# Optimization experiments

Hardware: AMD Instinct MI355X
Metric: run time of the kernel (lower is better)

## Reference

```python
import jax, jax.numpy as jnp
import numpy as np

D_MODEL = 1024
NUM_HEADS = 16
D_K = D_MODEL // NUM_HEADS


def setup_inputs() -> dict:
    key = jax.random.key(0)
    ks = jax.random.split(key, 12)
    B, S = 1, 4096
    s = 1.0 / np.sqrt(D_MODEL)
    inp = {
        'query': jax.random.normal(ks[0], (B, S, D_MODEL), jnp.float32),
        'key': jax.random.normal(ks[1], (B, S, D_MODEL), jnp.float32),
        'value': jax.random.normal(ks[2], (B, S, D_MODEL), jnp.float32),
        'W_q': jax.random.normal(ks[3], (D_MODEL, D_MODEL), jnp.float32) * s,
        'b_q': jnp.zeros((D_MODEL,), jnp.float32),
        'W_k': jax.random.normal(ks[4], (D_MODEL, D_MODEL), jnp.float32) * s,
        'b_k': jnp.zeros((D_MODEL,), jnp.float32),
        'W_v': jax.random.normal(ks[5], (D_MODEL, D_MODEL), jnp.float32) * s,
        'b_v': jnp.zeros((D_MODEL,), jnp.float32),
        'W_o': jax.random.normal(ks[6], (D_MODEL, D_MODEL), jnp.float32) * s,
        'b_o': jnp.zeros((D_MODEL,), jnp.float32),
    }
    return inp


def reference(query, key, value, W_q, b_q, W_k, b_k, W_v, b_v, W_o, b_o):
    B, S, _ = query.shape
    # torch nn.Linear: y = x @ W.T + b
    Q = query @ W_q.T + b_q
    K = key @ W_k.T + b_k
    V = value @ W_v.T + b_v
    # (B, S, H, d_k) -> (B, H, S, d_k)
    Q = Q.reshape(B, S, NUM_HEADS, D_K).transpose(0, 2, 1, 3)
    K = K.reshape(B, S, NUM_HEADS, D_K).transpose(0, 2, 1, 3)
    V = V.reshape(B, S, NUM_HEADS, D_K).transpose(0, 2, 1, 3)
    scale = 1.0 / jnp.sqrt(jnp.asarray(D_K, Q.dtype))
    qk = jnp.einsum('bhqd,bhkd->bhqk', Q, K) * scale  # [B,H,S,S]
    attn = jax.nn.softmax(qk, axis=-1)
    out = jnp.einsum('bhqk,bhkd->bhqd', attn, V)
    out = out.transpose(0, 2, 1, 3).reshape(B, S, D_MODEL)
    return out @ W_o.T + b_o
```

## Files before the change

### kernel.cpp

```cpp
#include <hip/hip_runtime.h>
#include <cstdint>
#include <cstddef>

typedef __bf16 bf16_t;
typedef _Float16 f16_t;
typedef __attribute__((ext_vector_type(8))) __bf16 bf16x8;
typedef __attribute__((ext_vector_type(4))) __bf16 bf16x4;
typedef __attribute__((ext_vector_type(2))) __bf16 bf16x2;
typedef __attribute__((ext_vector_type(8))) _Float16 f16x8;
typedef __attribute__((ext_vector_type(2))) _Float16 f16x2;
typedef __attribute__((ext_vector_type(4))) float floatx4;
typedef __attribute__((ext_vector_type(2))) float floatx2;
typedef __attribute__((ext_vector_type(16))) float floatx16;
typedef __attribute__((ext_vector_type(2))) int i32x2;

#define S_LEN 4096
#define DM 1024
#define NH 16
#define DKH 64
#define NSPLIT 4
#define KT_PER (S_LEN / 64 / NSPLIT)

#define QSCALE 0.1803368801111601f

__device__ __forceinline__ void async_b128(void* lds, const void* g) {
    __builtin_amdgcn_global_load_lds(
        (__attribute__((address_space(1))) void*)(uintptr_t)g,
        (__attribute__((address_space(3))) void*)lds,
        16, 0, 0);
}

__device__ __forceinline__ void fence_all() { __builtin_amdgcn_s_waitcnt(0); }

__device__ __forceinline__ floatx4 mfma16(bf16x8 a, bf16x8 b, floatx4 c) {
    return __builtin_amdgcn_mfma_f32_16x16x32_bf16(a, b, c, 0, 0, 0);
}
__device__ __forceinline__ floatx16 mfma32(bf16x8 a, bf16x8 b, floatx16 c) {
    return __builtin_amdgcn_mfma_f32_32x32x16_bf16(a, b, c, 0, 0, 0);
}
__device__ __forceinline__ int f2i(float x) { return __builtin_bit_cast(int, x); }
__device__ __forceinline__ float i2f(int x) { return __builtin_bit_cast(float, x); }
__device__ __forceinline__ int p2i(bf16x2 x) { return __builtin_bit_cast(int, x); }

__global__ __launch_bounds__(256) void convert_all_kernel(
    const float* __restrict__ q, const float* __restrict__ k,
    const float* __restrict__ v, const float* __restrict__ wqf,
    const float* __restrict__ wkf, const float* __restrict__ wvf,
    const float* __restrict__ wof, bf16_t* __restrict__ dst_in,
    bf16_t* __restrict__ dst_w) {
    const size_t i = ((size_t)blockIdx.x * 256 + threadIdx.x) * 4;
    const float* s;
    bf16_t* d;
    size_t off;
    if (i < 12582912) {
        const int r = (int)(i >> 22);
        s = (r == 0) ? q : (r == 1) ? k : v;
        off = i & 4194303;
        d = dst_in + (size_t)r * 4194304 + off;
    } else {
        const size_t j = i - 12582912;
        const int r = (int)(j >> 20);
        s = (r == 0) ? wqf : (r == 1) ? wkf : (r == 2) ? wvf : wof;
        off = j & 1048575;
        d = dst_w + (size_t)r * 1048576 + off;
    }
    const floatx4 val = *(const floatx4*)(s + off);
    bf16x4 o;
    o[0] = (bf16_t)val[0]; o[1] = (bf16_t)val[1];
    o[2] = (bf16_t)val[2]; o[3] = (bf16_t)val[3];
    *(bf16x4*)d = o;
}

template <int BN, typename OutT, bool TRANSC>
__device__ __forceinline__ void gemm_bt_body(const bf16_t* __restrict__ A,
                                             const bf16_t* __restrict__ B,
                                             const float* __restrict__ bias,
                                             OutT* __restrict__ C, float oscale) {
    constexpr int K = 1024, N = 1024, BK = 64;
    constexpr int NT = BN / 32;
    __shared__ bf16_t As[128 * BK];
    __shared__ bf16_t Bs[BN * BK];
    const int tid = threadIdx.x;
    const int wid = tid >> 6, lane = tid & 63;
    const int quad = lane >> 4, l16 = lane & 15;
    const int m0 = blockIdx.y * 128, n0 = blockIdx.x * BN;
    const int wm = (wid & 1) * 64, wn = (wid >> 1) * (BN / 2);

    floatx4 acc[4][NT] = {};

    for (int k0 = 0; k0 < K; k0 += BK) {
        __syncthreads();
#pragma unroll
        for (int i = 0; i < (128 * BK) / 2048; ++i) {
            const int c = (i << 8) + tid;
            const int row = c >> 3;
            const int ko = (c & 7) << 3;
            const int lb = ((i << 8) + (wid << 6)) << 3;
            async_b128(&As[lb], A + (size_t)(m0 + row) * K + k0 + ko);
        }
#pragma unroll
        for (int i = 0; i < (BN * BK) / 2048; ++i) {
            const int c = (i << 8) + tid;
            const int row = c >> 3;
            const int ko = (c & 7) << 3;
            const int lb = ((i << 8) + (wid << 6)) << 3;
            async_b128(&Bs[lb], B + (size_t)(n0 + row) * K + k0 + ko);
        }
        fence_all();
        __syncthreads();

#pragma unroll
        for (int kk = 0; kk < 2; ++kk) {
            bf16x8 af[4], bfr[NT];
#pragma unroll
            for (int t = 0; t < 4; ++t)
                af[t] = *(const bf16x8*)&As[(wm + t * 16 + l16) * BK + kk * 32 + quad * 8];
#pragma unroll
            for (int t = 0; t < NT; ++t)
                bfr[t] = *(const bf16x8*)&Bs[(wn + t * 16 + l16) * BK + kk * 32 + quad * 8];
#pragma unroll
            for (int mt = 0; mt < 4; ++mt)
#pragma unroll
                for (int nt = 0; nt < NT; ++nt)
                    acc[mt][nt] = mfma16(af[mt], bfr[nt], acc[mt][nt]);
        }
    }

#pragma unroll
    for (int mt = 0; mt < 4; ++mt)
#pragma unroll
        for (int nt = 0; nt < NT; ++nt) {
            const int col = n0 + wn + nt * 16 + l16;
            const float bv = bias[col];
            if constexpr (TRANSC) {
                const int row0 = m0 + wm + mt * 16 + quad * 4;
                bf16x4 o;
#pragma unroll
                for (int r = 0; r < 4; ++r)
                    o[r] = (bf16_t)((acc[mt][nt][r] + bv) * oscale);
                *(bf16x4*)&C[(size_t)col * S_LEN + row0] = o;
            } else {
#pragma unroll
                for (int r = 0; r < 4; ++r) {
                    const int row = m0 + wm + mt * 16 + quad * 4 + r;
                    C[(size_t)row * N + col] = (OutT)((acc[mt][nt][r] + bv) * oscale);
                }
            }
        }
}

__global__ __launch_bounds__(256) void gemm_qkv_kernel(
    const bf16_t* __restrict__ qx, const bf16_t* __restrict__ kx,
    const bf16_t* __restrict__ vx, const bf16_t* __restrict__ wq,
    const bf16_t* __restrict__ wk, const bf16_t* __restrict__ wv,
    const float* __restrict__ bq, const float* __restrict__ bk,
    const float* __restrict__ bv, bf16_t* __restrict__ Qp,
    bf16_t* __restrict__ Kp, bf16_t* __restrict__ Vt) {
    const int z = blockIdx.z;
    const bf16_t* A = (z == 0) ? qx : (z == 1) ? kx : vx;
    const bf16_t* B = (z == 0) ? wq : (z == 1) ? wk : wv;
    const float* bias = (z == 0) ? bq : (z == 1) ? bk : bv;
    if (z == 2) {
        gemm_bt_body<128, bf16_t, true>(A, B, bias, Vt, 1.0f);
    } else {
        bf16_t* C = (z == 0) ? Qp : Kp;
        gemm_bt_body<128, bf16_t, false>(A, B, bias, C, (z == 0) ? QSCALE : 1.0f);
    }
}

__global__ __launch_bounds__(256) void gemm_out_kernel(
    const bf16_t* __restrict__ AO, const bf16_t* __restrict__ wo,
    const float* __restrict__ bo, float* __restrict__ out) {
    gemm_bt_body<64, float, false>(AO, wo, bo, out, 1.0f);
}

__global__ __launch_bounds__(256, 2) void flash_kernel(
    const bf16_t* __restrict__ Q, const bf16_t* __restrict__ K,
    const bf16_t* __restrict__ Vt, f16_t* __restrict__ Opart,
    float* __restrict__ Lpart) {
    __shared__ bf16_t smem[16384];
    bf16_t* Ks = smem;
    bf16_t* Vs = smem + 8192;

    const int tid = threadIdx.x;
    const int wave = tid >> 6, lane = tid & 63;
    const int h32 = lane >> 5, c = lane & 31;
    const int head = blockIdx.y;
    const int sp = blockIdx.z;
    const int qbase = blockIdx.x * 256 + wave * 64;
    const int kv0 = sp * (S_LEN / NSPLIT);

    bf16x8 Qf[2][4];
#pragma unroll
    for (int nt = 0; nt < 2; ++nt)
#pragma unroll
        for (int s = 0; s < 4; ++s)
            Qf[nt][s] = *(const bf16x8*)(Q + (size_t)(qbase + nt * 32 + c) * DM +
                                         head * DKH + s * 16 + h32 * 8);

    floatx16 oa[2][2] = {};
    floatx2 la2[2][2] = {};

    const bf16_t* kptr = K + (size_t)(kv0 + lane) * DM + head * DKH + wave * 16;
    const bf16_t* vptr = Vt + (size_t)(head * DKH + lane) * S_LEN + kv0 + wave * 16;
    bf16_t* ksl = Ks + wave * 1024;
    bf16_t* vsl = Vs + wave * 1024;

    async_b128(ksl, kptr);       async_b128(ksl + 512, kptr + 8);
    async_b128(vsl, vptr);       async_b128(vsl + 512, vptr + 8);
    kptr += 64 * DM; vptr += 64;

    for (int kt = 0; kt < KT_PER; ++kt) {
        const int buf = kt & 1;
        fence_all();
        __syncthreads();
        if (kt + 1 < KT_PER) {
            bf16_t* kd = ksl + (buf ^ 1) * 4096;
            bf16_t* vd = vsl + (buf ^ 1) * 4096;
            async_b128(kd, kptr);     async_b128(kd + 512, kptr + 8);
            async_b128(vd, vptr);     async_b128(vd + 512, vptr + 8);
            kptr += 64 * DM; vptr += 64;
        }

        bf16x8 Kf[2][4];
#pragma unroll
        for (int mt = 0; mt < 2; ++mt)
#pragma unroll
            for (int s = 0; s < 4; ++s)
                Kf[mt][s] = *(const bf16x8*)&Ks[buf * 4096 + ((2 * s + h32) * 64 + mt * 32 + c) * 8];

        floatx16 sc[2][2];
#pragma unroll
        for (int mt = 0; mt < 2; ++mt)
#pragma unroll
            for (int nt = 0; nt < 2; ++nt)
#pragma unroll
                for (int j = 0; j < 16; ++j)
                    sc[mt][nt][j] = -3.0f;

#pragma unroll
        for (int s = 0; s < 4; ++s)
#pragma unroll
            for (int mt = 0; mt < 2; ++mt)
#pragma unroll
                for (int nt = 0; nt < 2; ++nt)
                    sc[mt][nt] = mfma32(Kf[mt][s], Qf[nt][s], sc[mt][nt]);

        bf16x8 Vf[2][4];
#pragma unroll
        for (int dt = 0; dt < 2; ++dt)
#pragma unroll
            for (int s = 0; s < 4; ++s)
                Vf[dt][s] = *(const bf16x8*)&Vs[buf * 4096 + ((2 * s + h32) * 64 + dt * 32 + c) * 8];

#pragma unroll
        for (int nt = 0; nt < 2; ++nt) {
            int pk[2][8];
#pragma unroll
            for (int mt = 0; mt < 2; ++mt)
#pragma unroll
                for (int rr = 0; rr < 8; ++rr) {
                    const float p0 = __builtin_amdgcn_exp2f(sc[mt][nt][2 * rr]);
                    const float p1 = __builtin_amdgcn_exp2f(sc[mt][nt][2 * rr + 1]);
                    la2[nt][rr & 1] += floatx2{p0, p1};
                    bf16x2 w; w[0] = (bf16_t)p0; w[1] = (bf16_t)p1;
                    pk[mt][rr] = p2i(w);
                }
#pragma unroll
            for (int s = 0; s < 4; ++s) {
                const int a = s >> 1, b4 = (s & 1) * 4;
                const i32x2 r02 = __builtin_amdgcn_permlane32_swap(
                    pk[a][b4 + 0], pk[a][b4 + 2], false, false);
                const i32x2 r13 = __builtin_amdgcn_permlane32_swap(
                    pk[a][b4 + 1], pk[a][b4 + 3], false, false);
                union { bf16x8 v; int d[4]; } P;
                P.d[0] = r02[0];
                P.d[1] = r13[0];
                P.d[2] = r02[1];
                P.d[3] = r13[1];
                oa[0][nt] = mfma32(Vf[0][s], P.v, oa[0][nt]);
                oa[1][nt] = mfma32(Vf[1][s], P.v, oa[1][nt]);
            }
        }
    }

#pragma unroll
    for (int nt = 0; nt < 2; ++nt) {
        float t = la2[nt][0][0] + la2[nt][0][1] + la2[nt][1][0] + la2[nt][1][1];
        t += i2f(__shfl_xor(f2i(t), 32));
        if (h32 == 0)
            Lpart[(size_t)(sp * NH + head) * S_LEN + qbase + nt * 32 + c] = t;
    }

    fence_all();
    __syncthreads();
    f16_t* ot = (f16_t*)smem + wave * (32 * 72);
#pragma unroll
    for (int nt = 0; nt < 2; ++nt) {
#pragma unroll
        for (int dt = 0; dt < 2; ++dt)
#pragma unroll
            for (int rr = 0; rr < 8; ++rr) {
                const int d0 = dt * 32 + ((2 * rr) & 3) + 8 * (rr >> 1) + 4 * h32;
                f16x2 w;
                w[0] = (f16_t)oa[dt][nt][2 * rr];
                w[1] = (f16_t)oa[dt][nt][2 * rr + 1];
                *(f16x2*)&ot[c * 72 + d0] = w;
            }
        fence_all();
        __syncthreads();
        const int r = lane & 31;
#pragma unroll
        for (int j = 0; j < 4; ++j) {
            const f16x8 v = *(const f16x8*)&ot[r * 72 + h32 * 32 + j * 8];
            *(f16x8*)(Opart + ((size_t)sp * S_LEN + qbase + nt * 32 + r) * DM +
                      head * DKH + h32 * 32 + j * 8) = v;
        }
        fence_all();
        __syncthreads();
    }
}

__global__ __launch_bounds__(256) void reduce_kernel(
    const f16_t* __restrict__ Op, const float* __restrict__ Lp,
    bf16_t* __restrict__ AO) {
    const size_t f = ((size_t)blockIdx.x * 256 + threadIdx.x) * 8;
    const int q = (int)(f >> 10);
    const int h = (int)((f & 1023) >> 6);
    float l = 0.f;
#pragma unroll
    for (int sp = 0; sp < NSPLIT; ++sp)
        l += Lp[(size_t)(sp * NH + h) * S_LEN + q];
    const float inv = 1.0f / l;
    float s[8] = {};
#pragma unroll
    for (int sp = 0; sp < NSPLIT; ++sp) {
        const f16x8 v = *(const f16x8*)(Op + (size_t)sp * (S_LEN * DM) + f);
#pragma unroll
        for (int j = 0; j < 8; ++j) s[j] += (float)v[j];
    }
    bf16x8 o;
#pragma unroll
    for (int j = 0; j < 8; ++j) o[j] = (bf16_t)(s[j] * inv);
    *(bf16x8*)(AO + f) = o;
}

extern "C" void kernel_launch(void* const* d_in, const int* in_sizes, int n_in,
                              void* d_out, int out_size, void* d_ws, size_t ws_size,
                              hipStream_t stream) {
    const float* q  = (const float*)d_in[0];
    const float* k  = (const float*)d_in[1];
    const float* v  = (const float*)d_in[2];
    const float* Wq = (const float*)d_in[3];
    const float* bq = (const float*)d_in[4];
    const float* Wk = (const float*)d_in[5];
    const float* bk = (const float*)d_in[6];
    const float* Wv = (const float*)d_in[7];
    const float* bv = (const float*)d_in[8];
    const float* Wo = (const float*)d_in[9];
    const float* bo = (const float*)d_in[10];
    float* out = (float*)d_out;

    bf16_t* ws = (bf16_t*)d_ws;
    bf16_t* qx = ws;
    bf16_t* kx = qx + 4194304;
    bf16_t* vx = kx + 4194304;
    bf16_t* spare = vx + 4194304;
    f16_t*  Opart = (f16_t*)ws;
    bf16_t* wq = spare + 4194304;
    bf16_t* wk = wq + 1048576;
    bf16_t* wv = wk + 1048576;
    bf16_t* wo = wv + 1048576;
    bf16_t* Qp = wo + 1048576;
    bf16_t* Kp = Qp + 4194304;
    bf16_t* Vt = Kp + 4194304;
    bf16_t* AO = Vt + 4194304;
    float*  Lpart = (float*)(AO + 4194304);

    convert_all_kernel<<<dim3(16384), 256, 0, stream>>>(q, k, v, Wq, Wk, Wv, Wo,
                                                        qx, wq);
    gemm_qkv_kernel<<<dim3(8, 32, 3), 256, 0, stream>>>(qx, kx, vx, wq, wk, wv,
                                                        bq, bk, bv, Qp, Kp, Vt);
    flash_kernel<<<dim3(16, 16, NSPLIT), 256, 0, stream>>>(Qp, Kp, Vt, Opart, Lpart);
    reduce_kernel<<<dim3(2048), 256, 0, stream>>>(Opart, Lpart, AO);
    gemm_out_kernel<<<dim3(16, 32), 256, 0, stream>>>(AO, wo, bo, out);
    (void)in_sizes; (void)n_in; (void)out_size; (void)ws_size;
}
```

Measured before the change: 268.9 us.

## Fuse fp32-to-bf16 input conversion into QKV GEMM tile loads

Removes the separate pass that converted the query/key/value activations to bf16. The QKV GEMM now loads fp32 tiles straight into LDS, using an XOR swizzle to avoid bank conflicts, and converts them to bf16 in registers before the MFMA. The K tile shrinks from 64 to 32 for every GEMM so the fp32 A tile fits in LDS, which doubles the number of barrier and load rounds per GEMM. Only the weights are still converted in a separate, smaller kernel.

```diff
diff --git a/kernel.cpp b/kernel.cpp
--- a/kernel.cpp
+++ b/kernel.cpp
@@ -42,43 +42,33 @@
 __device__ __forceinline__ float i2f(int x) { return __builtin_bit_cast(float, x); }
 __device__ __forceinline__ int p2i(bf16x2 x) { return __builtin_bit_cast(int, x); }
 
-__global__ __launch_bounds__(256) void convert_all_kernel(
-    const float* __restrict__ q, const float* __restrict__ k,
-    const float* __restrict__ v, const float* __restrict__ wqf,
-    const float* __restrict__ wkf, const float* __restrict__ wvf,
-    const float* __restrict__ wof, bf16_t* __restrict__ dst_in,
+__global__ __launch_bounds__(256) void convert_w_kernel(
+    const float* __restrict__ wqf, const float* __restrict__ wkf,
+    const float* __restrict__ wvf, const float* __restrict__ wof,
     bf16_t* __restrict__ dst_w) {
     const size_t i = ((size_t)blockIdx.x * 256 + threadIdx.x) * 4;
-    const float* s;
-    bf16_t* d;
-    size_t off;
-    if (i < 12582912) {
-        const int r = (int)(i >> 22);
-        s = (r == 0) ? q : (r == 1) ? k : v;
-        off = i & 4194303;
-        d = dst_in + (size_t)r * 4194304 + off;
-    } else {
-        const size_t j = i - 12582912;
-        const int r = (int)(j >> 20);
-        s = (r == 0) ? wqf : (r == 1) ? wkf : (r == 2) ? wvf : wof;
-        off = j & 1048575;
-        d = dst_w + (size_t)r * 1048576 + off;
-    }
+    const int r = (int)(i >> 20);
+    const float* s = (r == 0) ? wqf : (r == 1) ? wkf : (r == 2) ? wvf : wof;
+    const size_t off = i & 1048575;
     const floatx4 val = *(const floatx4*)(s + off);
     bf16x4 o;
     o[0] = (bf16_t)val[0]; o[1] = (bf16_t)val[1];
     o[2] = (bf16_t)val[2]; o[3] = (bf16_t)val[3];
-    *(bf16x4*)d = o;
-}
-
-template <int BN, typename OutT, bool TRANSC>
-__device__ __forceinline__ void gemm_bt_body(const bf16_t* __restrict__ A,
+    *(bf16x4*)(dst_w + (size_t)r * 1048576 + off) = o;
+}
+
+template <int BN, typename OutT, bool TRANSC, typename AT>
+__device__ __forceinline__ void gemm_bt_body(const AT* __restrict__ A,
                                              const bf16_t* __restrict__ B,
                                              const float* __restrict__ bias,
                                              OutT* __restrict__ C, float oscale) {
-    constexpr int K = 1024, N = 1024, BK = 64;
+    constexpr int K = 1024, N = 1024, BK = 32;
     constexpr int NT = BN / 32;
-    __shared__ bf16_t As[128 * BK];
+    constexpr bool AF32 = (sizeof(AT) == 4);
+    constexpr int ECH = 16 / sizeof(AT);
+    constexpr int CPR = BK / ECH;
+    constexpr int NCH = (128 * BK) / ECH / 256;
+    __shared__ AT As[128 * BK];
     __shared__ bf16_t Bs[BN * BK];
     const int tid = threadIdx.x;
     const int wid = tid >> 6, lane = tid & 63;
@@ -91,39 +81,57 @@
     for (int k0 = 0; k0 < K; k0 += BK) {
         __syncthreads();
 #pragma unroll
-        for (int i = 0; i < (128 * BK) / 2048; ++i) {
+        for (int i = 0; i < NCH; ++i) {
             const int c = (i << 8) + tid;
-            const int row = c >> 3;
-            const int ko = (c & 7) << 3;
-            const int lb = ((i << 8) + (wid << 6)) << 3;
-            async_b128(&As[lb], A + (size_t)(m0 + row) * K + k0 + ko);
+            const int row = c / CPR;
+            int cidx = c % CPR;
+            if constexpr (AF32) cidx ^= (row & 7);
+            const int lb = ((i << 8) + (wid << 6)) * ECH;
+            async_b128(&As[lb], A + (size_t)(m0 + row) * K + k0 + cidx * ECH);
         }
 #pragma unroll
         for (int i = 0; i < (BN * BK) / 2048; ++i) {
             const int c = (i << 8) + tid;
-            const int row = c >> 3;
-            const int ko = (c & 7) << 3;
+            const int row = c >> 2;
+            const int ko = (c & 3) << 3;
             const int lb = ((i << 8) + (wid << 6)) << 3;
             async_b128(&Bs[lb], B + (size_t)(n0 + row) * K + k0 + ko);
         }
         fence_all();
         __syncthreads();
 
-#pragma unroll
-        for (int kk = 0; kk < 2; ++kk) {
-            bf16x8 af[4], bfr[NT];
+        bf16x8 af[4], bfr[NT];
+        if constexpr (AF32) {
+            const float* Afp = (const float*)As;
+#pragma unroll
+            for (int t = 0; t < 4; ++t) {
+                const int r = wm + t * 16 + l16;
+                const int r7 = r & 7;
+                const floatx4 f0 = *(const floatx4*)
+                    &Afp[r * BK + ((((quad << 1) | 0) ^ r7) << 2)];
+                const floatx4 f1 = *(const floatx4*)
+                    &Afp[r * BK + ((((quad << 1) | 1) ^ r7) << 2)];
+                bf16x8 a;
+#pragma unroll
+                for (int j = 0; j < 4; ++j) {
+                    a[j] = (bf16_t)f0[j];
+                    a[4 + j] = (bf16_t)f1[j];
+                }
+                af[t] = a;
+            }
+        } else {
 #pragma unroll
             for (int t = 0; t < 4; ++t)
-                af[t] = *(const bf16x8*)&As[(wm + t * 16 + l16) * BK + kk * 32 + quad * 8];
-#pragma unroll
-            for (int t = 0; t < NT; ++t)
-                bfr[t] = *(const bf16x8*)&Bs[(wn + t * 16 + l16) * BK + kk * 32 + quad * 8];
-#pragma unroll
-            for (int mt = 0; mt < 4; ++mt)
-#pragma unroll
-                for (int nt = 0; nt < NT; ++nt)
-                    acc[mt][nt] = mfma16(af[mt], bfr[nt], acc[mt][nt]);
-        }
+                af[t] = *(const bf16x8*)&As[(wm + t * 16 + l16) * BK + quad * 8];
+        }
+#pragma unroll
+        for (int t = 0; t < NT; ++t)
+            bfr[t] = *(const bf16x8*)&Bs[(wn + t * 16 + l16) * BK + quad * 8];
+#pragma unroll
+        for (int mt = 0; mt < 4; ++mt)
+#pragma unroll
+            for (int nt = 0; nt < NT; ++nt)
+                acc[mt][nt] = mfma16(af[mt], bfr[nt], acc[mt][nt]);
     }
 
 #pragma unroll
@@ -150,28 +158,29 @@
 }
 
 __global__ __launch_bounds__(256) void gemm_qkv_kernel(
-    const bf16_t* __restrict__ qx, const bf16_t* __restrict__ kx,
-    const bf16_t* __restrict__ vx, const bf16_t* __restrict__ wq,
+    const float* __restrict__ q, const float* __restrict__ k,
+    const float* __restrict__ v, const bf16_t* __restrict__ wq,
     const bf16_t* __restrict__ wk, const bf16_t* __restrict__ wv,
     const float* __restrict__ bq, const float* __restrict__ bk,
     const float* __restrict__ bv, bf16_t* __restrict__ Qp,
     bf16_t* __restrict__ Kp, bf16_t* __restrict__ Vt) {
     const int z = blockIdx.z;
-    const bf16_t* A = (z == 0) ? qx : (z == 1) ? kx : vx;
+    const float* A = (z == 0) ? q : (z == 1) ? k : v;
     const bf16_t* B = (z == 0) ? wq : (z == 1) ? wk : wv;
     const float* bias = (z == 0) ? bq : (z == 1) ? bk : bv;
     if (z == 2) {
-        gemm_bt_body<128, bf16_t, true>(A, B, bias, Vt, 1.0f);
+        gemm_bt_body<128, bf16_t, true, float>(A, B, bias, Vt, 1.0f);
     } else {
         bf16_t* C = (z == 0) ? Qp : Kp;
-        gemm_bt_body<128, bf16_t, false>(A, B, bias, C, (z == 0) ? QSCALE : 1.0f);
+        gemm_bt_body<128, bf16_t, false, float>(A, B, bias, C,
+                                                (z == 0) ? QSCALE : 1.0f);
     }
 }
 
 __global__ __launch_bounds__(256) void gemm_out_kernel(
     const bf16_t* __restrict__ AO, const bf16_t* __restrict__ wo,
     const float* __restrict__ bo, float* __restrict__ out) {
-    gemm_bt_body<64, float, false>(AO, wo, bo, out, 1.0f);
+    gemm_bt_body<64, float, false, bf16_t>(AO, wo, bo, out, 1.0f);
 }
 
 __global__ __launch_bounds__(256, 2) void flash_kernel(
@@ -362,12 +371,8 @@
     float* out = (float*)d_out;
 
     bf16_t* ws = (bf16_t*)d_ws;
-    bf16_t* qx = ws;
-    bf16_t* kx = qx + 4194304;
-    bf16_t* vx = kx + 4194304;
-    bf16_t* spare = vx + 4194304;
     f16_t*  Opart = (f16_t*)ws;
-    bf16_t* wq = spare + 4194304;
+    bf16_t* wq = ws + 16777216;
     bf16_t* wk = wq + 1048576;
     bf16_t* wv = wk + 1048576;
     bf16_t* wo = wv + 1048576;
@@ -377,9 +382,8 @@
     bf16_t* AO = Vt + 4194304;
     float*  Lpart = (float*)(AO + 4194304);
 
-    convert_all_kernel<<<dim3(16384), 256, 0, stream>>>(q, k, v, Wq, Wk, Wv, Wo,
-                                                        qx, wq);
-    gemm_qkv_kernel<<<dim3(8, 32, 3), 256, 0, stream>>>(qx, kx, vx, wq, wk, wv,
+    convert_w_kernel<<<dim3(4096), 256, 0, stream>>>(Wq, Wk, Wv, Wo, wq);
+    gemm_qkv_kernel<<<dim3(8, 32, 3), 256, 0, stream>>>(q, k, v, wq, wk, wv,
                                                         bq, bk, bv, Qp, Kp, Vt);
     flash_kernel<<<dim3(16, 16, NSPLIT), 256, 0, stream>>>(Qp, Kp, Vt, Opart, Lpart);
     reduce_kernel<<<dim3(2048), 256, 0, stream>>>(Opart, Lpart, AO);
```

Result: no change. 268.9 us (-0.0%).
